# Optimization experiments

Measured on AMD Instinct MI355X. Metric: run time of the kernel, lower is better.

The kernel has to match this reference:

```python
import jax, jax.numpy as jnp
import numpy as np

D_MODEL = 1024
H = 16
DK = 64  # d_model // h
M = 8    # memory slots
NQ = 1024
B = 8


def setup_inputs() -> dict:
    key = jax.random.key(0)
    ks = jax.random.split(key, 10)
    f = lambda k, s, sc=1.0: jax.random.normal(k, s, dtype=jnp.float32) * sc
    return {
        "queries": f(ks[0], (NQ, B, D_MODEL)),
        "keys": f(ks[1], (NQ, B, D_MODEL)),
        "values": f(ks[2], (NQ, B, D_MODEL)),
        "m_k": f(ks[3], (1, M, D_MODEL), 0.1),
        "m_v": f(ks[4], (1, M, D_MODEL), 0.1),
        "attn_mask": f(ks[5], (B, H, NQ, NQ), 0.02),  # additive float mask over real keys
        "in_proj_weight": f(ks[6], (3 * D_MODEL, D_MODEL), 0.02),
        "in_proj_bias": jnp.zeros((3 * D_MODEL,), jnp.float32),
        "out_w": f(ks[7], (D_MODEL, D_MODEL), 0.02),
        "out_b": jnp.zeros((D_MODEL,), jnp.float32),
    }


def _fp16(w):
    # The torch module casts projection weights/biases to fp16 before linear.
    return w.astype(jnp.float16).astype(jnp.float32)


def reference(queries, keys, values, m_k, m_v, attn_mask,
              in_proj_weight, in_proj_bias, out_w, out_b):
    # (seq, batch, d) -> (batch, seq, d)
    q_in = queries.transpose(1, 0, 2)
    k_in = keys.transpose(1, 0, 2)
    v_in = values.transpose(1, 0, 2)
    b, nq, d = q_in.shape
    nk = k_in.shape[1]
    m = m_k.shape[1]

    w_q, w_k, w_v = jnp.split(in_proj_weight, 3, axis=0)
    b_q, b_k, b_v = jnp.split(in_proj_bias, 3)

    q = q_in @ _fp16(w_q).T + _fp16(b_q)
    k = k_in @ _fp16(w_k).T + _fp16(b_k)
    v = v_in @ _fp16(w_v).T + _fp16(b_v)

    # scaled learnable memory slots, broadcast over batch
    mk = float(np.sqrt(DK * H)) * jnp.broadcast_to(m_k, (b, m, d))
    mv = float(np.sqrt(m)) * jnp.broadcast_to(m_v, (b, m, d))
    k = jnp.concatenate([k, mk], axis=1)  # (b, nk+m, d)
    v = jnp.concatenate([v, mv], axis=1)

    qh = q.reshape(b, nq, H, DK).transpose(0, 2, 1, 3)        # (b,h,nq,dk)
    kh = k.reshape(b, nk + m, H, DK).transpose(0, 2, 3, 1)    # (b,h,dk,nk+m)
    vh = v.reshape(b, nk + m, H, DK).transpose(0, 2, 1, 3)    # (b,h,nk+m,dv)

    att = jnp.matmul(qh, kh) / float(np.sqrt(DK))             # (b,h,nq,nk+m)
    # additive mask applies only to the real keys, memory slots unmasked
    mask_pad = jnp.concatenate(
        [attn_mask, jnp.zeros((b, H, nq, m), att.dtype)], axis=-1)
    att = jax.nn.softmax(att + mask_pad, axis=-1)

    out = jnp.matmul(att, vh).transpose(0, 2, 1, 3).reshape(b, nq, H * DK)
    out = out @ out_w.T + out_b
    return out.transpose(1, 0, 2)  # back to (seq, batch, d)
```

## Files before the change

### kernel.cpp

```cpp
#include <hip/hip_runtime.h>
#include <cstdint>

typedef _Float16 half8  __attribute__((ext_vector_type(8)));
typedef _Float16 half4v __attribute__((ext_vector_type(4)));
typedef float    f32x4  __attribute__((ext_vector_type(4)));

#define MFMA_F16(a,b,c) __builtin_amdgcn_mfma_f32_16x16x32_f16(a,b,c,0,0,0)

static constexpr int D = 1024, H = 16, DK = 64, BATCH = 8, NQ = 1024;
static constexpr int NKP = 1040;

__device__ __forceinline__ void async_copy16(_Float16* lds, const _Float16* g) {
  __builtin_amdgcn_global_load_lds(
      (const __attribute__((address_space(1))) void*)g,
      (__attribute__((address_space(3))) void*)lds, 16, 0, 0);
}

__global__ __launch_bounds__(256) void convert_all(
    const float* __restrict__ q, const float* __restrict__ k, const float* __restrict__ v,
    const float* __restrict__ w_in, const float* __restrict__ w_out,
    _Float16* __restrict__ q16, _Float16* __restrict__ k16, _Float16* __restrict__ v16,
    _Float16* __restrict__ win16, _Float16* __restrict__ wout16)
{
  const unsigned NA = 8192u * 1024u;
  const unsigned NW = 3u * 1024u * 1024u;
  unsigned idx = blockIdx.x * 256u + threadIdx.x;
  unsigned e = idx * 8u;
  const float* src;
  _Float16* dst;
  unsigned off;
  if (e < NA)            { src = q;     dst = q16;    off = e; }
  else if (e < 2 * NA)   { src = k;     dst = k16;    off = e - NA; }
  else if (e < 3 * NA)   { src = v;     dst = v16;    off = e - 2 * NA; }
  else if (e < 3 * NA + NW) { src = w_in; dst = win16; off = e - 3 * NA; }
  else                   { src = w_out; dst = wout16; off = e - 3 * NA - NW; }
  float4 f0 = ((const float4*)(src + off))[0];
  float4 f1 = ((const float4*)(src + off))[1];
  half8 h;
  h[0]=(_Float16)f0.x; h[1]=(_Float16)f0.y; h[2]=(_Float16)f0.z; h[3]=(_Float16)f0.w;
  h[4]=(_Float16)f1.x; h[5]=(_Float16)f1.y; h[6]=(_Float16)f1.z; h[7]=(_Float16)f1.w;
  *(half8*)(dst + off) = h;
}

__global__ __launch_bounds__(256) void gemm_qkv(
    const _Float16* __restrict__ A16,
    const _Float16* __restrict__ W16,
    const float* __restrict__ bias,
    _Float16* __restrict__ Qo, _Float16* __restrict__ Ko, _Float16* __restrict__ Vo)
{
  const int z = blockIdx.z;
  const _Float16* __restrict__ A = A16 + (size_t)z * 8192 * 1024;
  const _Float16* __restrict__ Wz = W16 + (size_t)z * D * D;
  const int row0 = blockIdx.x * 128;
  const int col0 = blockIdx.y * 128;

  __shared__ _Float16 As[128 * 64];
  __shared__ _Float16 Bs[128 * 64];

  const int tid = threadIdx.x;
  const int wv = tid >> 6, lane = tid & 63, c = lane & 15, g = lane >> 4;
  const int ar0 = (wv & 1) * 64, bc0 = (wv >> 1) * 64;
  const int cswz = (c & 7) << 3;

  const int srow = tid >> 3;
  const int sk8 = (((tid & 7) ^ ((tid >> 3) & 7)) << 3);
  const _Float16* ag = A + (size_t)(row0 + srow) * D + sk8;
  const _Float16* bg = Wz + (size_t)(col0 + srow) * D + sk8;
  _Float16* al = &As[512 * wv];
  _Float16* bl = &Bs[512 * wv];

  f32x4 acc[4][4];
#pragma unroll
  for (int i = 0; i < 4; i++)
#pragma unroll
    for (int j = 0; j < 4; j++) acc[i][j] = (f32x4)(0.f);

  for (int kb = 0; kb < D; kb += 64) {
#pragma unroll
    for (int u = 0; u < 4; u++) {
      async_copy16(al + 2048 * u, ag + kb + (size_t)(32 * u) * D);
      async_copy16(bl + 2048 * u, bg + kb + (size_t)(32 * u) * D);
    }
    __syncthreads();
#pragma unroll
    for (int kk = 0; kk < 2; kk++) {
      half8 af[4], bf[4];
#pragma unroll
      for (int i = 0; i < 4; i++)
        af[i] = *(const half8*)&As[(ar0 + 16 * i + c) * 64 + ((32 * kk + 8 * g) ^ cswz)];
#pragma unroll
      for (int j = 0; j < 4; j++)
        bf[j] = *(const half8*)&Bs[(bc0 + 16 * j + c) * 64 + ((32 * kk + 8 * g) ^ cswz)];
#pragma unroll
      for (int i = 0; i < 4; i++)
#pragma unroll
        for (int j = 0; j < 4; j++) acc[i][j] = MFMA_F16(af[i], bf[j], acc[i][j]);
    }
    __syncthreads();
  }

#pragma unroll
  for (int j = 0; j < 4; j++) {
    int n = col0 + bc0 + 16 * j + c;
    float bb = (float)(_Float16)bias[z * D + n];
    int h_ = n >> 6, dk = n & 63;
#pragma unroll
    for (int i = 0; i < 4; i++) {
#pragma unroll
      for (int r = 0; r < 4; r++) {
        int m = row0 + ar0 + 16 * i + 4 * g + r;
        int b = m & 7, nq = m >> 3;
        float val = acc[i][j][r] + bb;
        if (z == 0)
          Qo[(((size_t)b * H + h_) * NQ + nq) * DK + dk] = (_Float16)(val * 0.125f);
        else if (z == 1)
          Ko[(((size_t)b * H + h_) * NKP + nq) * DK + dk] = (_Float16)val;
        else
          Vo[(((size_t)b * H + h_) * NKP + nq) * DK + dk] = (_Float16)val;
      }
    }
  }
}

__global__ __launch_bounds__(256) void fill_slots(
    const float* __restrict__ mk, const float* __restrict__ mv,
    _Float16* __restrict__ Ko, _Float16* __restrict__ Vo)
{
  int idx = blockIdx.x * 256 + threadIdx.x;
  int which = idx >> 17;
  int e = idx & 131071;
  int dk = e & 63, r = (e >> 6) & 15, h = (e >> 10) & 15, b = (e >> 14) & 7;
  float val = 0.f;
  if (r < 8) {
    int src = r * D + h * DK + dk;
    val = which ? 2.8284271247461903f * mv[src] : 32.f * mk[src];
  }
  _Float16* dst = which ? Vo : Ko;
  dst[(((size_t)b * H + h) * NKP + 1024 + r) * DK + dk] = (_Float16)val;
}

__global__ __launch_bounds__(512) void attn(
    const _Float16* __restrict__ Qg, const _Float16* __restrict__ Kg,
    const _Float16* __restrict__ Vg, const float* __restrict__ mask,
    _Float16* __restrict__ Hid)
{
  const int qt = blockIdx.x;
  const int bh = blockIdx.y;
  const int b = bh >> 4, h = bh & 15;
  const int tid = threadIdx.x;
  const int wv = tid >> 6, lane = tid & 63, c = lane & 15, g = lane >> 4;

  __shared__ _Float16 QPs[128 * 72];
  __shared__ _Float16 Ks[64 * 72];
  __shared__ _Float16 Vt[64 * 72];

  const _Float16* qbase = Qg + ((size_t)bh * NQ + qt * 128) * DK;
#pragma unroll
  for (int u = 0; u < 2; u++) {
    int id = tid + 512 * u;
    int row = id >> 3, m8 = (id & 7) * 8;
    *(int4*)&QPs[row * 72 + m8] = *(const int4*)(qbase + row * DK + m8);
  }
  __syncthreads();
  const int qrow = (wv * 16 + c) * 72;
  half8 qf0 = *(const half8*)&QPs[qrow + 8 * g];
  half8 qf1 = *(const half8*)&QPs[qrow + 32 + 8 * g];

  f32x4 oacc[4];
#pragma unroll
  for (int j = 0; j < 4; j++) oacc[j] = (f32x4)(0.f);
  float lpart = 0.f;

  const float* maskbase = mask + ((size_t)bh << 20) + ((size_t)(qt * 128 + wv * 16 + c) << 10);
  const _Float16* kbase_g = Kg + (size_t)bh * NKP * DK;
  const _Float16* vbase_g = Vg + (size_t)bh * NKP * DK;

  for (int ci = 0; ci < 17; ++ci) {
    const int kb = ci * 64;
    const int nk = (ci < 16) ? 64 : 16;
    __syncthreads();

    f32x4 sinit[4];
    if (ci < 16) {
#pragma unroll
      for (int t = 0; t < 4; t++)
        sinit[t] = *(const f32x4*)(maskbase + kb + 16 * t + 4 * g);
    } else {
      float iv = (g < 2) ? 0.f : -1e30f;
      sinit[0] = (f32x4){iv, iv, iv, iv};
    }

    {
      int row = tid >> 3, m8 = (tid & 7) * 8;
      if (row < nk)
        *(int4*)&Ks[row * 72 + m8] = *(const int4*)(kbase_g + (size_t)(kb + row) * DK + m8);
    }
    if (tid < 256) {
      int kp = tid & 31, dvo = (tid >> 5) * 8;
      if (2 * kp < nk) {
        uint4 a4 = *(const uint4*)(vbase_g + (size_t)(kb + 2 * kp) * DK + dvo);
        uint4 b4 = *(const uint4*)(vbase_g + (size_t)(kb + 2 * kp + 1) * DK + dvo);
        uint32_t aw[4] = {a4.x, a4.y, a4.z, a4.w};
        uint32_t bw[4] = {b4.x, b4.y, b4.z, b4.w};
#pragma unroll
        for (int w = 0; w < 4; w++) {
          uint32_t lo = (aw[w] & 0xffffu) | (bw[w] << 16);
          uint32_t hi = (aw[w] >> 16) | (bw[w] & 0xffff0000u);
          *(uint32_t*)&Vt[(dvo + 2 * w) * 72 + 2 * kp] = lo;
          *(uint32_t*)&Vt[(dvo + 2 * w + 1) * 72 + 2 * kp] = hi;
        }
      } else if (nk == 16) {
#pragma unroll
        for (int w = 0; w < 4; w++) {
          *(uint32_t*)&Vt[(dvo + 2 * w) * 72 + 2 * kp] = 0u;
          *(uint32_t*)&Vt[(dvo + 2 * w + 1) * 72 + 2 * kp] = 0u;
        }
      }
    }
    __syncthreads();

    const int ntile = nk >> 4;
    for (int t = 0; t < ntile; ++t) {
      f32x4 s = sinit[t];
      half8 kf0 = *(const half8*)&Ks[(16 * t + c) * 72 + 8 * g];
      half8 kf1 = *(const half8*)&Ks[(16 * t + c) * 72 + 32 + 8 * g];
      s = MFMA_F16(kf0, qf0, s);
      s = MFMA_F16(kf1, qf1, s);
      f32x4 p;
      p[0] = __expf(s[0]); p[1] = __expf(s[1]); p[2] = __expf(s[2]); p[3] = __expf(s[3]);
      lpart += p[0] + p[1] + p[2] + p[3];
      half4v ph;
      ph[0] = (_Float16)p[0]; ph[1] = (_Float16)p[1];
      ph[2] = (_Float16)p[2]; ph[3] = (_Float16)p[3];
      *(half4v*)&QPs[qrow + 16 * t + 4 * g] = ph;
    }
    if (nk == 16) {
      half4v zz = {(_Float16)0, (_Float16)0, (_Float16)0, (_Float16)0};
      *(half4v*)&QPs[qrow + 16 + 4 * g] = zz;
    }

    const int khalf = (nk == 64) ? 2 : 1;
    for (int kh = 0; kh < khalf; ++kh) {
      half8 pf = *(const half8*)&QPs[qrow + 32 * kh + 8 * g];
#pragma unroll
      for (int j = 0; j < 4; j++) {
        half8 vf = *(const half8*)&Vt[(16 * j + c) * 72 + 32 * kh + 8 * g];
        oacc[j] = MFMA_F16(pf, vf, oacc[j]);
      }
    }
  }

  lpart += __shfl_xor(lpart, 16);
  lpart += __shfl_xor(lpart, 32);
  float inv_[4];
#pragma unroll
  for (int r = 0; r < 4; r++) {
    float lq = __shfl(lpart, 4 * g + r);
    inv_[r] = __builtin_amdgcn_rcpf(lq);
  }
#pragma unroll
  for (int j = 0; j < 4; j++) {
    int col = h * DK + 16 * j + c;
#pragma unroll
    for (int r = 0; r < 4; r++) {
      int q = qt * 128 + wv * 16 + 4 * g + r;
      Hid[((size_t)q * BATCH + b) * D + col] = (_Float16)(oacc[j][r] * inv_[r]);
    }
  }
}

__global__ __launch_bounds__(256) void gemm_out(
    const _Float16* __restrict__ Ah, const _Float16* __restrict__ W16,
    const float* __restrict__ bias, float* __restrict__ Out)
{
  const int row0 = blockIdx.x * 128, col0 = blockIdx.y * 128;
  __shared__ _Float16 As[128 * 64];
  __shared__ _Float16 Bs[128 * 64];
  const int tid = threadIdx.x;
  const int wv = tid >> 6, lane = tid & 63, c = lane & 15, g = lane >> 4;
  const int ar0 = (wv & 1) * 64, bc0 = (wv >> 1) * 64;
  const int cswz = (c & 7) << 3;

  const int srow = tid >> 3;
  const int sk8 = (((tid & 7) ^ ((tid >> 3) & 7)) << 3);
  const _Float16* ag = Ah + (size_t)(row0 + srow) * D + sk8;
  const _Float16* bg = W16 + (size_t)(col0 + srow) * D + sk8;
  _Float16* al = &As[512 * wv];
  _Float16* bl = &Bs[512 * wv];

  f32x4 acc[4][4];
#pragma unroll
  for (int i = 0; i < 4; i++)
#pragma unroll
    for (int j = 0; j < 4; j++) acc[i][j] = (f32x4)(0.f);

  for (int kb = 0; kb < D; kb += 64) {
#pragma unroll
    for (int u = 0; u < 4; u++) {
      async_copy16(al + 2048 * u, ag + kb + (size_t)(32 * u) * D);
      async_copy16(bl + 2048 * u, bg + kb + (size_t)(32 * u) * D);
    }
    __syncthreads();
#pragma unroll
    for (int kk = 0; kk < 2; kk++) {
      half8 af[4], bf[4];
#pragma unroll
      for (int i = 0; i < 4; i++)
        af[i] = *(const half8*)&As[(ar0 + 16 * i + c) * 64 + ((32 * kk + 8 * g) ^ cswz)];
#pragma unroll
      for (int j = 0; j < 4; j++)
        bf[j] = *(const half8*)&Bs[(bc0 + 16 * j + c) * 64 + ((32 * kk + 8 * g) ^ cswz)];
#pragma unroll
      for (int i = 0; i < 4; i++)
#pragma unroll
        for (int j = 0; j < 4; j++) acc[i][j] = MFMA_F16(af[i], bf[j], acc[i][j]);
    }
    __syncthreads();
  }

#pragma unroll
  for (int j = 0; j < 4; j++) {
    int n = col0 + bc0 + 16 * j + c;
    float bb = bias[n];
#pragma unroll
    for (int i = 0; i < 4; i++) {
#pragma unroll
      for (int r = 0; r < 4; r++) {
        int m = row0 + ar0 + 16 * i + 4 * g + r;
        Out[(size_t)m * D + n] = acc[i][j][r] + bb;
      }
    }
  }
}

extern "C" void kernel_launch(void* const* d_in, const int* in_sizes, int n_in,
                              void* d_out, int out_size, void* d_ws, size_t ws_size,
                              hipStream_t stream) {
  const float* queries   = (const float*)d_in[0];
  const float* keys      = (const float*)d_in[1];
  const float* values    = (const float*)d_in[2];
  const float* m_k       = (const float*)d_in[3];
  const float* m_v       = (const float*)d_in[4];
  const float* attn_mask = (const float*)d_in[5];
  const float* in_proj_w = (const float*)d_in[6];
  const float* in_proj_b = (const float*)d_in[7];
  const float* out_w     = (const float*)d_in[8];
  const float* out_b     = (const float*)d_in[9];
  float* out = (float*)d_out;

  const size_t NA = (size_t)8192 * 1024;
  _Float16* A16  = (_Float16*)d_ws;
  _Float16* Win16  = A16 + 3 * NA;
  _Float16* Wout16 = Win16 + (size_t)3 * 1024 * 1024;
  _Float16* Qw = Wout16 + (size_t)1024 * 1024;
  _Float16* Kw = Qw + (size_t)8 * 16 * 1024 * 64;
  _Float16* Vw = Kw + (size_t)8 * 16 * 1040 * 64;
  _Float16* Hw = Vw + (size_t)8 * 16 * 1040 * 64;

  hipLaunchKernelGGL(convert_all, dim3(14336), dim3(256), 0, stream,
                     queries, keys, values, in_proj_w, out_w,
                     A16, A16 + NA, A16 + 2 * NA, Win16, Wout16);
  hipLaunchKernelGGL(gemm_qkv, dim3(64, 8, 3), dim3(256), 0, stream,
                     A16, Win16, in_proj_b, Qw, Kw, Vw);
  hipLaunchKernelGGL(fill_slots, dim3(1024), dim3(256), 0, stream, m_k, m_v, Kw, Vw);
  hipLaunchKernelGGL(attn, dim3(8, 128), dim3(512), 0, stream, Qw, Kw, Vw, attn_mask, Hw);
  hipLaunchKernelGGL(gemm_out, dim3(64, 8), dim3(256), 0, stream, Hw, Wout16, out_b, out);
}
```

Measured before the change: 932.4 us.

## Prefetch next K/V/mask chunk into registers during attention compute

Software-pipelines the attention loop: the global loads for the next 64-key chunk of K, V and the additive mask are issued into registers right after the LDS barrier, so their latency overlaps the current chunk's MFMA and exp work. The loop start then only stores the registers into LDS. It also raises wave priority around the MFMA groups with s_setprio. This costs extra registers per thread, which may lower occupancy at 512 threads per block.

```diff
diff --git a/kernel.cpp b/kernel.cpp
--- a/kernel.cpp
+++ b/kernel.cpp
@@ -155,6 +155,26 @@
   __shared__ _Float16 Vt[64 * 72];
 
   const _Float16* qbase = Qg + ((size_t)bh * NQ + qt * 128) * DK;
+  const float* maskbase = mask + ((size_t)bh << 20) + ((size_t)(qt * 128 + wv * 16 + c) << 10);
+  const _Float16* kbase_g = Kg + (size_t)bh * NKP * DK;
+  const _Float16* vbase_g = Vg + (size_t)bh * NKP * DK;
+
+  const int krow = tid >> 3;
+  const int km8  = (tid & 7) * 8;
+  const int vkp  = tid & 31;
+  const int vdvo = (tid >> 5) * 8;
+
+  int4 kreg = *(const int4*)(kbase_g + (size_t)krow * DK + km8);
+  uint4 va, vb;
+  if (tid < 256) {
+    va = *(const uint4*)(vbase_g + (size_t)(2 * vkp) * DK + vdvo);
+    vb = *(const uint4*)(vbase_g + (size_t)(2 * vkp + 1) * DK + vdvo);
+  }
+  f32x4 sinit[4];
+#pragma unroll
+  for (int t = 0; t < 4; t++)
+    sinit[t] = *(const f32x4*)(maskbase + 16 * t + 4 * g);
+
 #pragma unroll
   for (int u = 0; u < 2; u++) {
     int id = tid + 512 * u;
@@ -171,61 +191,63 @@
   for (int j = 0; j < 4; j++) oacc[j] = (f32x4)(0.f);
   float lpart = 0.f;
 
-  const float* maskbase = mask + ((size_t)bh << 20) + ((size_t)(qt * 128 + wv * 16 + c) << 10);
-  const _Float16* kbase_g = Kg + (size_t)bh * NKP * DK;
-  const _Float16* vbase_g = Vg + (size_t)bh * NKP * DK;
-
   for (int ci = 0; ci < 17; ++ci) {
-    const int kb = ci * 64;
     const int nk = (ci < 16) ? 64 : 16;
     __syncthreads();
 
-    f32x4 sinit[4];
-    if (ci < 16) {
-#pragma unroll
-      for (int t = 0; t < 4; t++)
-        sinit[t] = *(const f32x4*)(maskbase + kb + 16 * t + 4 * g);
-    } else {
-      float iv = (g < 2) ? 0.f : -1e30f;
-      sinit[0] = (f32x4){iv, iv, iv, iv};
-    }
-
-    {
-      int row = tid >> 3, m8 = (tid & 7) * 8;
-      if (row < nk)
-        *(int4*)&Ks[row * 72 + m8] = *(const int4*)(kbase_g + (size_t)(kb + row) * DK + m8);
-    }
+    if (krow < nk)
+      *(int4*)&Ks[krow * 72 + km8] = kreg;
     if (tid < 256) {
-      int kp = tid & 31, dvo = (tid >> 5) * 8;
-      if (2 * kp < nk) {
-        uint4 a4 = *(const uint4*)(vbase_g + (size_t)(kb + 2 * kp) * DK + dvo);
-        uint4 b4 = *(const uint4*)(vbase_g + (size_t)(kb + 2 * kp + 1) * DK + dvo);
-        uint32_t aw[4] = {a4.x, a4.y, a4.z, a4.w};
-        uint32_t bw[4] = {b4.x, b4.y, b4.z, b4.w};
+      if (2 * vkp < nk) {
+        uint32_t aw[4] = {va.x, va.y, va.z, va.w};
+        uint32_t bw[4] = {vb.x, vb.y, vb.z, vb.w};
 #pragma unroll
         for (int w = 0; w < 4; w++) {
           uint32_t lo = (aw[w] & 0xffffu) | (bw[w] << 16);
           uint32_t hi = (aw[w] >> 16) | (bw[w] & 0xffff0000u);
-          *(uint32_t*)&Vt[(dvo + 2 * w) * 72 + 2 * kp] = lo;
-          *(uint32_t*)&Vt[(dvo + 2 * w + 1) * 72 + 2 * kp] = hi;
+          *(uint32_t*)&Vt[(vdvo + 2 * w) * 72 + 2 * vkp] = lo;
+          *(uint32_t*)&Vt[(vdvo + 2 * w + 1) * 72 + 2 * vkp] = hi;
         }
       } else if (nk == 16) {
 #pragma unroll
         for (int w = 0; w < 4; w++) {
-          *(uint32_t*)&Vt[(dvo + 2 * w) * 72 + 2 * kp] = 0u;
-          *(uint32_t*)&Vt[(dvo + 2 * w + 1) * 72 + 2 * kp] = 0u;
+          *(uint32_t*)&Vt[(vdvo + 2 * w) * 72 + 2 * vkp] = 0u;
+          *(uint32_t*)&Vt[(vdvo + 2 * w + 1) * 72 + 2 * vkp] = 0u;
         }
       }
     }
     __syncthreads();
+
+    f32x4 scur[4];
+    scur[0] = sinit[0]; scur[1] = sinit[1]; scur[2] = sinit[2]; scur[3] = sinit[3];
+    if (ci < 16) {
+      const int kbn = (ci + 1) * 64;
+      const int nkn = (ci + 1 < 16) ? 64 : 16;
+      if (krow < nkn)
+        kreg = *(const int4*)(kbase_g + (size_t)(kbn + krow) * DK + km8);
+      if (tid < 256 && 2 * vkp < nkn) {
+        va = *(const uint4*)(vbase_g + (size_t)(kbn + 2 * vkp) * DK + vdvo);
+        vb = *(const uint4*)(vbase_g + (size_t)(kbn + 2 * vkp + 1) * DK + vdvo);
+      }
+      if (ci + 1 < 16) {
+#pragma unroll
+        for (int t = 0; t < 4; t++)
+          sinit[t] = *(const f32x4*)(maskbase + kbn + 16 * t + 4 * g);
+      } else {
+        float iv = (g < 2) ? 0.f : -1e30f;
+        sinit[0] = (f32x4){iv, iv, iv, iv};
+      }
+    }
 
     const int ntile = nk >> 4;
     for (int t = 0; t < ntile; ++t) {
-      f32x4 s = sinit[t];
+      f32x4 s = scur[t];
       half8 kf0 = *(const half8*)&Ks[(16 * t + c) * 72 + 8 * g];
       half8 kf1 = *(const half8*)&Ks[(16 * t + c) * 72 + 32 + 8 * g];
+      __builtin_amdgcn_s_setprio(1);
       s = MFMA_F16(kf0, qf0, s);
       s = MFMA_F16(kf1, qf1, s);
+      __builtin_amdgcn_s_setprio(0);
       f32x4 p;
       p[0] = __expf(s[0]); p[1] = __expf(s[1]); p[2] = __expf(s[2]); p[3] = __expf(s[3]);
       lpart += p[0] + p[1] + p[2] + p[3];
@@ -242,11 +264,13 @@
     const int khalf = (nk == 64) ? 2 : 1;
     for (int kh = 0; kh < khalf; ++kh) {
       half8 pf = *(const half8*)&QPs[qrow + 32 * kh + 8 * g];
+      __builtin_amdgcn_s_setprio(1);
 #pragma unroll
       for (int j = 0; j < 4; j++) {
         half8 vf = *(const half8*)&Vt[(16 * j + c) * 72 + 32 * kh + 8 * g];
         oacc[j] = MFMA_F16(pf, vf, oacc[j]);
       }
+      __builtin_amdgcn_s_setprio(0);
     }
   }
 
```

Result: no change. 914.8 us (-1.9%).
